# Performance work log

Measured on AMD Instinct MI355X. Metric: run time of the kernel, lower is better.

## Reference

```python
import jax, jax.numpy as jnp
import numpy as np

N_NODES = 100000
N_EDGES = 1600000
NFEAT, NHID, NCLASS = 256, 128, 40


def setup_inputs() -> dict:
    key = jax.random.key(0)
    ks = jax.random.split(key, 8)
    x = jax.random.normal(ks[0], (N_NODES, NFEAT), dtype=jnp.float32)
    edge_src = jax.random.randint(ks[1], (N_EDGES,), 0, N_NODES, dtype=jnp.int32)
    edge_dst = jax.random.randint(ks[2], (N_EDGES,), 0, N_NODES, dtype=jnp.int32)
    edge_weight = jax.random.uniform(ks[3], (N_EDGES,), dtype=jnp.float32)
    W1 = jax.random.normal(ks[4], (NFEAT, NHID), dtype=jnp.float32) * (1.0 / np.sqrt(NFEAT))
    b1 = jnp.zeros((NHID,), dtype=jnp.float32)
    W2 = jax.random.normal(ks[5], (NHID, NCLASS), dtype=jnp.float32) * (1.0 / np.sqrt(NHID))
    b2 = jnp.zeros((NCLASS,), dtype=jnp.float32)
    return {"x": x, "edge_src": edge_src, "edge_dst": edge_dst,
            "edge_weight": edge_weight, "W1": W1, "b1": b1, "W2": W2, "b2": b2}


def _spmm(edge_src, edge_dst, edge_weight, h):
    # out[i] = sum_{e: dst[e]==i} w[e] * h[src[e]]  (sparse adj @ h)
    msgs = edge_weight[:, None] * h[edge_src]            # [E, D]
    return jax.ops.segment_sum(msgs, edge_dst, num_segments=N_NODES)


def reference(x, edge_src, edge_dst, edge_weight, W1, b1, W2, b2):
    # GraphConvolution 1: adj @ (x @ W1) + b1, then ReLU
    h = _spmm(edge_src, edge_dst, edge_weight, x @ W1) + b1
    h = jax.nn.relu(h)
    # Dropout(p=0.5) is identity in eval/deterministic reference
    # GraphConvolution 2: adj @ (h @ W2) + b2
    out = _spmm(edge_src, edge_dst, edge_weight, h @ W2) + b2
    return out
```

## Files before the change

kernel.cpp:

```cpp
#include <hip/hip_runtime.h>

#define N_NODES 100000
#define N_EDGES 1600000
#define NFEAT 256
#define NHID 128
#define NCLASS 40

#define NGROUP 8
#define NODES_PER_GROUP 12500
#define NBKT 128
#define NPB 782
#define KPB (NPB * 8)
#define BCAP2 13200
#define EPB2 8192
#define NCH2 ((N_EDGES + EPB2 - 1) / EPB2)
#define NGEMM1 ((N_NODES + 127) / 128)
#define NKEY (N_NODES * 8)

using short8 = __attribute__((ext_vector_type(8))) short;
using f32x4 = __attribute__((ext_vector_type(4))) float;
using i32x4 = __attribute__((ext_vector_type(4))) int;
using i32x2 = __attribute__((ext_vector_type(2))) int;

__device__ inline float blo(unsigned u) { return __uint_as_float(u << 16); }
__device__ inline float bhi(unsigned u) { return __uint_as_float(u & 0xffff0000u); }
__device__ inline unsigned pk2(float a, float b) {
  unsigned x = __float_as_uint(a), y = __float_as_uint(b);
  unsigned lo = (x + 0x7FFFu + ((x >> 16) & 1u)) >> 16;
  unsigned hi = (y + 0x7FFFu + ((y >> 16) & 1u)) >> 16;
  return lo | (hi << 16);
}
__device__ inline unsigned short pk1(float a) {
  unsigned x = __float_as_uint(a);
  return (unsigned short)((x + 0x7FFFu + ((x >> 16) & 1u)) >> 16);
}


__global__ __launch_bounds__(512) void k_fatA(const int* __restrict__ src,
                                              const int* __restrict__ dst,
                                              const float* __restrict__ w,
                                              int* __restrict__ bcnt,
                                              int* __restrict__ bktK,
                                              i32x2* __restrict__ bktSW,
                                              const float* __restrict__ W1,
                                              unsigned short* __restrict__ w1s) {
  int tid = threadIdx.x;
  if (blockIdx.x >= NCH2) {
    int t = (blockIdx.x - NCH2) * 512 + tid;
    if (t < NFEAT * NHID) {
      int k = t >> 7, c = t & 127;
      int idx = (c * 256 + k) ^ ((c & 7) << 3);
      w1s[idx] = pk1(W1[t]);
    }
    return;
  }
  __shared__ int lcnt[NBKT], loff[NBKT], lcur[NBKT], lbase[NBKT];
  __shared__ int eK[EPB2];
  __shared__ i32x2 eSW[EPB2];
  if (tid < NBKT) lcnt[tid] = 0;
  __syncthreads();

  int base_e = blockIdx.x * EPB2;
  int nE = N_EDGES - base_e;
  if (nE > EPB2) nE = EPB2;
  int e0 = base_e + tid * 16;
  int key[16];
  i32x2 sw[16];
  bool full = (tid * 16 + 16 <= nE);
  if (full) {
#pragma unroll
    for (int g = 0; g < 4; g++) {
      i32x4 d4 = __builtin_nontemporal_load((const i32x4*)(dst + e0 + g * 4));
      i32x4 s4 = __builtin_nontemporal_load((const i32x4*)(src + e0 + g * 4));
      f32x4 w4 = __builtin_nontemporal_load((const f32x4*)(w + e0 + g * 4));
      int dd[4] = {d4.x, d4.y, d4.z, d4.w};
      int ss[4] = {s4.x, s4.y, s4.z, s4.w};
      float ww[4] = {w4.x, w4.y, w4.z, w4.w};
#pragma unroll
      for (int i = 0; i < 4; i++) {
        key[g * 4 + i] = dd[i] * 8 + (int)((unsigned)ss[i] / NODES_PER_GROUP);
        sw[g * 4 + i].x = ss[i];
        sw[g * 4 + i].y = __float_as_int(ww[i]);
        atomicAdd(&lcnt[(unsigned)dd[i] / NPB], 1);
      }
    }
  } else {
#pragma unroll
    for (int i = 0; i < 16; i++) {
      int e = tid * 16 + i;
      if (e < nE) {
        int d = dst[base_e + e], s = src[base_e + e];
        float ww = w[base_e + e];
        key[i] = d * 8 + (int)((unsigned)s / NODES_PER_GROUP);
        sw[i].x = s;
        sw[i].y = __float_as_int(ww);
        atomicAdd(&lcnt[(unsigned)d / NPB], 1);
      } else {
        key[i] = -1;
      }
    }
  }
  __syncthreads();
  if (tid < NBKT) loff[tid] = lcnt[tid];
  __syncthreads();
  for (int off = 1; off < NBKT; off <<= 1) {
    int u = (tid < NBKT && tid >= off) ? loff[tid - off] : 0;
    __syncthreads();
    if (tid < NBKT) loff[tid] += u;
    __syncthreads();
  }
  if (tid < NBKT) {
    int excl = loff[tid] - lcnt[tid];
    loff[tid] = excl;
    lcur[tid] = excl;
    lbase[tid] = atomicAdd(&bcnt[tid], lcnt[tid]);
  }
  __syncthreads();
#pragma unroll
  for (int i = 0; i < 16; i++) {
    if (key[i] >= 0) {
      int b = (unsigned)key[i] / KPB;
      int p = atomicAdd(&lcur[b], 1);
      eK[p] = key[i];
      eSW[p] = sw[i];
    }
  }
  __syncthreads();
  int wid = tid >> 6, lane = tid & 63;
  for (int b = wid; b < NBKT; b += 8) {
    int cnt = lcnt[b];
    int l0 = loff[b];
    int gb = lbase[b];
    if (gb + cnt > BCAP2) cnt = BCAP2 - gb;
    size_t g0 = (size_t)b * BCAP2 + gb;
    for (int i = lane; i < cnt; i += 64) {
      bktK[g0 + i] = eK[l0 + i];
      bktSW[g0 + i] = eSW[l0 + i];
    }
  }
}


__global__ __launch_bounds__(256) void k_gemm1(const float* __restrict__ x,
                                               const uint4* __restrict__ w1s,
                                               unsigned* __restrict__ h1u) {
  __shared__ char sB[65536];
  int tid = threadIdx.x;
  {
    uint4* dd = (uint4*)sB;
    for (int i = 0; i < 16; i++) dd[tid + i * 256] = w1s[tid + i * 256];
  }
  __syncthreads();

  int lane = tid & 63, wid = tid >> 6;
  int r16 = lane & 15, kgrp = lane >> 4;
  int rowbase = blockIdx.x * 128 + wid * 32;
  int ra0 = min(rowbase + r16, N_NODES - 1);
  int ra1 = min(rowbase + 16 + r16, N_NODES - 1);

  f32x4 acc[2][8];
#pragma unroll
  for (int m = 0; m < 2; m++)
#pragma unroll
    for (int n = 0; n < 8; n++) acc[m][n] = (f32x4){0.f, 0.f, 0.f, 0.f};

  for (int kt8 = 0; kt8 < 8; kt8++) {
    int k0 = kt8 * 32 + kgrp * 8;
    union { uint4 u; short8 s; } a[2];
#pragma unroll
    for (int m = 0; m < 2; m++) {
      const float* ap = x + (size_t)(m ? ra1 : ra0) * NFEAT + k0;
      float4 v0 = *(const float4*)ap;
      float4 v1 = *(const float4*)(ap + 4);
      a[m].u.x = pk2(v0.x, v0.y);
      a[m].u.y = pk2(v0.z, v0.w);
      a[m].u.z = pk2(v1.x, v1.y);
      a[m].u.w = pk2(v1.z, v1.w);
    }
#pragma unroll
    for (int n = 0; n < 8; n++) {
      int c = 16 * n + r16;
      int off = (c * 512 + k0 * 2) ^ ((c & 7) << 4);
      short8 b = *(const short8*)(sB + off);
      acc[0][n] = __builtin_amdgcn_mfma_f32_16x16x32_bf16(a[0].s, b, acc[0][n], 0, 0, 0);
      acc[1][n] = __builtin_amdgcn_mfma_f32_16x16x32_bf16(a[1].s, b, acc[1][n], 0, 0, 0);
    }
  }

#pragma unroll
  for (int m = 0; m < 2; m++) {
    int rb = rowbase + m * 16 + kgrp * 4;
#pragma unroll
    for (int n = 0; n < 8; n++) {
      f32x4 v = acc[m][n];
#pragma unroll
      for (int j = 0; j < 4; j++) {
        float o = __shfl_xor(v[j], 1);
        int row = rb + j;
        if (!(lane & 1) && row < N_NODES)
          h1u[(size_t)row * 64 + 8 * n + (r16 >> 1)] = pk2(v[j], o);
      }
    }
  }
}


__global__ __launch_bounds__(1024) void k_build(const int* __restrict__ bcnt,
                                                const int* __restrict__ bktK,
                                                const i32x2* __restrict__ bktSW,
                                                int* __restrict__ rp2,
                                                i32x2* __restrict__ esw) {
  __shared__ int lh[KPB];
  __shared__ int partial[1024];
  __shared__ int sc[NBKT];
  __shared__ i32x2 ebuf[BCAP2];

  int b = blockIdx.x;
  int t = threadIdx.x;
  if (t < NBKT) sc[t] = bcnt[t];
  __syncthreads();
  for (int off = 1; off < NBKT; off <<= 1) {
    int u = (t < NBKT && t >= off) ? sc[t - off] : 0;
    __syncthreads();
    if (t < NBKT) sc[t] += u;
    __syncthreads();
  }
  int base = (b == 0) ? 0 : sc[b - 1];
  int cnt = min(bcnt[b], BCAP2);
  const int* kb = bktK + (size_t)b * BCAP2;
  const i32x2* sb = bktSW + (size_t)b * BCAP2;
  int k0 = b * KPB;

  for (int i = t; i < KPB; i += 1024) lh[i] = 0;
  __syncthreads();
  for (int i = t; i < cnt; i += 1024) atomicAdd(&lh[kb[i] - k0], 1);
  __syncthreads();

  int myoff = t * 7;
  int vals[7];
  int s0 = 0;
#pragma unroll
  for (int q = 0; q < 7; q++) {
    int i = myoff + q;
    int v = (i < KPB) ? lh[i] : 0;
    vals[q] = s0;
    s0 += v;
  }
  partial[t] = s0;
  __syncthreads();
  for (int off = 1; off < 1024; off <<= 1) {
    int u = (t >= off) ? partial[t - off] : 0;
    __syncthreads();
    partial[t] += u;
    __syncthreads();
  }
  int excl_base = partial[t] - s0;
  __syncthreads();
#pragma unroll
  for (int q = 0; q < 7; q++) {
    int i = myoff + q;
    if (i < KPB) {
      int e = excl_base + vals[q];
      int gk = k0 + i;
      if (gk < NKEY) rp2[gk] = base + e;
    }
  }
  __syncthreads();
#pragma unroll
  for (int q = 0; q < 7; q++) {
    int i = myoff + q;
    if (i < KPB) lh[i] = excl_base + vals[q];
  }
  if (b == NBKT - 1 && t == 0) rp2[NKEY] = N_EDGES;
  __syncthreads();

  for (int i = t; i < cnt; i += 1024) {
    int lk = kb[i] - k0;
    int pos = atomicAdd(&lh[lk], 1);
    ebuf[pos] = sb[i];
  }
  __syncthreads();

  i32x2* dstp = esw + base;
  for (int i = t; i < cnt; i += 1024) dstp[i] = ebuf[i];
}


__global__ __launch_bounds__(256) void k_spmm1(const unsigned* __restrict__ h1u,
                                               const int* __restrict__ rp2,
                                               const i32x2* __restrict__ esw,
                                               const float* __restrict__ bias1,
                                               unsigned* __restrict__ houtu) {
  int node = (blockIdx.x * 256 + threadIdx.x) >> 6;
  int lane = threadIdx.x & 63;
  if (node >= N_NODES) return;
  int beg = rp2[node * 8], end = rp2[node * 8 + 8];
  float aL0 = 0.f, aL1 = 0.f, aL2 = 0.f, aL3 = 0.f;
  float aH0 = 0.f, aH1 = 0.f, aH2 = 0.f, aH3 = 0.f;
  int j = beg;
  for (; j + 15 < end; j += 16) {
    i32x2 e[16];
#pragma unroll
    for (int q = 0; q < 16; q++) e[q] = esw[j + q];
    unsigned u[16];
#pragma unroll
    for (int q = 0; q < 16; q++) u[q] = h1u[((unsigned)e[q].x << 6) + lane];
#pragma unroll
    for (int q = 0; q < 16; q += 4) {
      float w0 = __int_as_float(e[q].y), w1 = __int_as_float(e[q + 1].y);
      float w2 = __int_as_float(e[q + 2].y), w3 = __int_as_float(e[q + 3].y);
      aL0 = fmaf(w0, blo(u[q]), aL0);     aH0 = fmaf(w0, bhi(u[q]), aH0);
      aL1 = fmaf(w1, blo(u[q + 1]), aL1); aH1 = fmaf(w1, bhi(u[q + 1]), aH1);
      aL2 = fmaf(w2, blo(u[q + 2]), aL2); aH2 = fmaf(w2, bhi(u[q + 2]), aH2);
      aL3 = fmaf(w3, blo(u[q + 3]), aL3); aH3 = fmaf(w3, bhi(u[q + 3]), aH3);
    }
  }
  for (; j + 7 < end; j += 8) {
    i32x2 e0 = esw[j],     e1 = esw[j + 1], e2 = esw[j + 2], e3 = esw[j + 3];
    i32x2 e4 = esw[j + 4], e5 = esw[j + 5], e6 = esw[j + 6], e7 = esw[j + 7];
    unsigned u0 = h1u[((unsigned)e0.x << 6) + lane];
    unsigned u1 = h1u[((unsigned)e1.x << 6) + lane];
    unsigned u2 = h1u[((unsigned)e2.x << 6) + lane];
    unsigned u3 = h1u[((unsigned)e3.x << 6) + lane];
    unsigned u4 = h1u[((unsigned)e4.x << 6) + lane];
    unsigned u5 = h1u[((unsigned)e5.x << 6) + lane];
    unsigned u6 = h1u[((unsigned)e6.x << 6) + lane];
    unsigned u7 = h1u[((unsigned)e7.x << 6) + lane];
    float w0 = __int_as_float(e0.y), w1 = __int_as_float(e1.y);
    float w2 = __int_as_float(e2.y), w3 = __int_as_float(e3.y);
    float w4 = __int_as_float(e4.y), w5 = __int_as_float(e5.y);
    float w6 = __int_as_float(e6.y), w7 = __int_as_float(e7.y);
    aL0 = fmaf(w0, blo(u0), aL0); aH0 = fmaf(w0, bhi(u0), aH0);
    aL1 = fmaf(w1, blo(u1), aL1); aH1 = fmaf(w1, bhi(u1), aH1);
    aL2 = fmaf(w2, blo(u2), aL2); aH2 = fmaf(w2, bhi(u2), aH2);
    aL3 = fmaf(w3, blo(u3), aL3); aH3 = fmaf(w3, bhi(u3), aH3);
    aL0 = fmaf(w4, blo(u4), aL0); aH0 = fmaf(w4, bhi(u4), aH0);
    aL1 = fmaf(w5, blo(u5), aL1); aH1 = fmaf(w5, bhi(u5), aH1);
    aL2 = fmaf(w6, blo(u6), aL2); aH2 = fmaf(w6, bhi(u6), aH2);
    aL3 = fmaf(w7, blo(u7), aL3); aH3 = fmaf(w7, bhi(u7), aH3);
  }
  for (; j + 3 < end; j += 4) {
    i32x2 e0 = esw[j], e1 = esw[j + 1], e2 = esw[j + 2], e3 = esw[j + 3];
    unsigned u0 = h1u[((unsigned)e0.x << 6) + lane];
    unsigned u1 = h1u[((unsigned)e1.x << 6) + lane];
    unsigned u2 = h1u[((unsigned)e2.x << 6) + lane];
    unsigned u3 = h1u[((unsigned)e3.x << 6) + lane];
    float w0 = __int_as_float(e0.y), w1 = __int_as_float(e1.y);
    float w2 = __int_as_float(e2.y), w3 = __int_as_float(e3.y);
    aL0 = fmaf(w0, blo(u0), aL0); aH0 = fmaf(w0, bhi(u0), aH0);
    aL1 = fmaf(w1, blo(u1), aL1); aH1 = fmaf(w1, bhi(u1), aH1);
    aL2 = fmaf(w2, blo(u2), aL2); aH2 = fmaf(w2, bhi(u2), aH2);
    aL3 = fmaf(w3, blo(u3), aL3); aH3 = fmaf(w3, bhi(u3), aH3);
  }
  for (; j < end; j++) {
    i32x2 e0 = esw[j];
    unsigned u0 = h1u[((unsigned)e0.x << 6) + lane];
    float w0 = __int_as_float(e0.y);
    aL0 = fmaf(w0, blo(u0), aL0); aH0 = fmaf(w0, bhi(u0), aH0);
  }
  float r0 = (aL0 + aL1) + (aL2 + aL3) + bias1[2 * lane];
  float r1 = (aH0 + aH1) + (aH2 + aH3) + bias1[2 * lane + 1];
  houtu[(size_t)node * 64 + lane] = pk2(fmaxf(r0, 0.f), fmaxf(r1, 0.f));
}


__global__ __launch_bounds__(256) void k_gemm2(const unsigned* __restrict__ h_u,
                                               const float* __restrict__ W2,
                                               unsigned short* __restrict__ h2b) {
  __shared__ float hs[32][132];
  __shared__ float w2t[40][132];
  int tid = threadIdx.x;
  int row0 = blockIdx.x * 32;
  for (int i = tid; i < NHID * NCLASS; i += 256) {
    int k = i / NCLASS, c = i % NCLASS;
    w2t[c][k] = W2[i];
  }
  for (int i = tid; i < 2048; i += 256) {
    int r = i >> 6, c = i & 63;
    unsigned u = h_u[(size_t)(row0 + r) * 64 + c];
    hs[r][2 * c] = blo(u);
    hs[r][2 * c + 1] = bhi(u);
  }
  __syncthreads();
  int r = tid >> 3;
  int c0 = (tid & 7) * 5;
  float acc[5] = {0, 0, 0, 0, 0};
  for (int k = 0; k < NHID; k += 4) {
    float4 a = *(float4*)&hs[r][k];
#pragma unroll
    for (int j = 0; j < 5; j++) {
      float4 b = *(float4*)&w2t[c0 + j][k];
      acc[j] += a.x * b.x + a.y * b.y + a.z * b.z + a.w * b.w;
    }
  }
#pragma unroll
  for (int j = 0; j < 5; j++) h2b[(size_t)(row0 + r) * NCLASS + c0 + j] = pk1(acc[j]);
}


__global__ __launch_bounds__(256) void k_spmm2(const unsigned* __restrict__ h2u,
                                               const int* __restrict__ rp2,
                                               const i32x2* __restrict__ esw,
                                               const float* __restrict__ b2,
                                               float* __restrict__ out) {
  int node = (blockIdx.x * 256 + threadIdx.x) >> 6;
  int lane = threadIdx.x & 63;
  if (node >= N_NODES) return;
  int beg = rp2[node * 8], end = rp2[node * 8 + 8];
  int g = lane / 20;
  int jj = lane - g * 20;
  float aA0 = 0.f, aB0 = 0.f, aA1 = 0.f, aB1 = 0.f;
  if (g < 3) {
    int e = beg + g;
    for (; e + 3 < end; e += 6) {
      i32x2 p0 = esw[e];
      i32x2 p1 = esw[e + 3];
      unsigned u0 = h2u[(size_t)p0.x * 20 + jj];
      unsigned u1 = h2u[(size_t)p1.x * 20 + jj];
      float w0 = __int_as_float(p0.y), w1 = __int_as_float(p1.y);
      aA0 = fmaf(w0, blo(u0), aA0); aB0 = fmaf(w0, bhi(u0), aB0);
      aA1 = fmaf(w1, blo(u1), aA1); aB1 = fmaf(w1, bhi(u1), aB1);
    }
    if (e < end) {
      i32x2 p0 = esw[e];
      unsigned u0 = h2u[(size_t)p0.x * 20 + jj];
      float w0 = __int_as_float(p0.y);
      aA0 = fmaf(w0, blo(u0), aA0); aB0 = fmaf(w0, bhi(u0), aB0);
    }
  }
  float accA = aA0 + aA1, accB = aB0 + aB1;
  float tA = accA + __shfl(accA, lane + 20) + __shfl(accA, lane + 40);
  float tB = accB + __shfl(accB, lane + 20) + __shfl(accB, lane + 40);
  if (lane < 20) {
    float2 o = make_float2(tA + b2[2 * lane], tB + b2[2 * lane + 1]);
    *(float2*)&out[(size_t)node * NCLASS + 2 * lane] = o;
  }
}

extern "C" void kernel_launch(void* const* d_in, const int* in_sizes, int n_in,
                              void* d_out, int out_size, void* d_ws, size_t ws_size,
                              hipStream_t stream) {
  const float* x = (const float*)d_in[0];
  const int* src_in = (const int*)d_in[1];
  const int* dst_in = (const int*)d_in[2];
  const float* w_in = (const float*)d_in[3];
  const float* W1 = (const float*)d_in[4];
  const float* b1 = (const float*)d_in[5];
  const float* W2 = (const float*)d_in[6];
  const float* b2 = (const float*)d_in[7];
  float* out = (float*)d_out;

  unsigned short* h1b = (unsigned short*)d_ws;
  unsigned* hbuf = (unsigned*)(h1b + (size_t)N_NODES * NHID);
  unsigned short* h2b = (unsigned short*)(hbuf + (size_t)N_NODES * 64);
  i32x2* esw = (i32x2*)(h2b + (size_t)N_NODES * NCLASS);
  i32x2* bktSW = esw + N_EDGES;
  int* bktK = (int*)(bktSW + (size_t)NBKT * BCAP2);
  int* bcnt = bktK + (size_t)NBKT * BCAP2;
  int* rp2 = bcnt + NBKT;
  unsigned short* w1s = (unsigned short*)(rp2 + NKEY + 4);

  hipMemsetAsync(bcnt, 0, NBKT * sizeof(int), stream);
  k_fatA<<<NCH2 + 64, 512, 0, stream>>>(src_in, dst_in, w_in, bcnt, bktK, bktSW, W1, w1s);
  k_gemm1<<<NGEMM1, 256, 0, stream>>>(x, (const uint4*)w1s, (unsigned*)h1b);
  k_build<<<NBKT, 1024, 0, stream>>>(bcnt, bktK, bktSW, rp2, esw);

  k_spmm1<<<(N_NODES + 3) / 4, 256, 0, stream>>>((const unsigned*)h1b, rp2, esw, b1, hbuf);
  k_gemm2<<<N_NODES / 32, 256, 0, stream>>>(hbuf, W2, h2b);
  k_spmm2<<<(N_NODES + 3) / 4, 256, 0, stream>>>((const unsigned*)h2b, rp2, esw, b2, out);
}
```

Before: 224.3 us.

## Fuse second-layer GEMM into first SpMM epilogue

The first SpMM kernel now keeps each node's ReLU'd hidden row in shared memory and immediately multiplies it by W2, which is staged into shared memory per block. It writes packed bf16 class logits directly, eliminating the separate GEMM kernel and the intermediate hidden-feature buffer round trip through global memory. In exchange, every block reloads the full 20KB W2 matrix and uses more shared memory, which may reduce occupancy in the gather-bound SpMM.

```diff
diff --git a/kernel.cpp b/kernel.cpp
--- a/kernel.cpp
+++ b/kernel.cpp
@@ -286,13 +286,24 @@
 }
 
 
-__global__ __launch_bounds__(256) void k_spmm1(const unsigned* __restrict__ h1u,
-                                               const int* __restrict__ rp2,
-                                               const i32x2* __restrict__ esw,
-                                               const float* __restrict__ bias1,
-                                               unsigned* __restrict__ houtu) {
-  int node = (blockIdx.x * 256 + threadIdx.x) >> 6;
-  int lane = threadIdx.x & 63;
+__global__ __launch_bounds__(256) void k_spmm1f(const unsigned* __restrict__ h1u,
+                                                const int* __restrict__ rp2,
+                                                const i32x2* __restrict__ esw,
+                                                const float* __restrict__ bias1,
+                                                const float* __restrict__ W2,
+                                                unsigned* __restrict__ h2u) {
+  __shared__ float w2s[NHID * NCLASS];
+  __shared__ float hrow[4][NHID];
+  int tid = threadIdx.x;
+  {
+    float4* d4 = (float4*)w2s;
+    const float4* s4 = (const float4*)W2;
+    for (int i = tid; i < NHID * NCLASS / 4; i += 256) d4[i] = s4[i];
+  }
+  __syncthreads();
+
+  int node = (blockIdx.x * 256 + tid) >> 6;
+  int lane = tid & 63, wid = tid >> 6;
   if (node >= N_NODES) return;
   int beg = rp2[node * 8], end = rp2[node * 8 + 8];
   float aL0 = 0.f, aL1 = 0.f, aL2 = 0.f, aL3 = 0.f;
@@ -360,41 +371,23 @@
   }
   float r0 = (aL0 + aL1) + (aL2 + aL3) + bias1[2 * lane];
   float r1 = (aH0 + aH1) + (aH2 + aH3) + bias1[2 * lane + 1];
-  houtu[(size_t)node * 64 + lane] = pk2(fmaxf(r0, 0.f), fmaxf(r1, 0.f));
-}
-
-
-__global__ __launch_bounds__(256) void k_gemm2(const unsigned* __restrict__ h_u,
-                                               const float* __restrict__ W2,
-                                               unsigned short* __restrict__ h2b) {
-  __shared__ float hs[32][132];
-  __shared__ float w2t[40][132];
-  int tid = threadIdx.x;
-  int row0 = blockIdx.x * 32;
-  for (int i = tid; i < NHID * NCLASS; i += 256) {
-    int k = i / NCLASS, c = i % NCLASS;
-    w2t[c][k] = W2[i];
-  }
-  for (int i = tid; i < 2048; i += 256) {
-    int r = i >> 6, c = i & 63;
-    unsigned u = h_u[(size_t)(row0 + r) * 64 + c];
-    hs[r][2 * c] = blo(u);
-    hs[r][2 * c + 1] = bhi(u);
-  }
-  __syncthreads();
-  int r = tid >> 3;
-  int c0 = (tid & 7) * 5;
-  float acc[5] = {0, 0, 0, 0, 0};
+  hrow[wid][2 * lane] = fmaxf(r0, 0.f);
+  hrow[wid][2 * lane + 1] = fmaxf(r1, 0.f);
+
+  int c = lane < NCLASS ? lane : NCLASS - 1;
+  float acc = 0.f;
+#pragma unroll 8
   for (int k = 0; k < NHID; k += 4) {
-    float4 a = *(float4*)&hs[r][k];
-#pragma unroll
-    for (int j = 0; j < 5; j++) {
-      float4 b = *(float4*)&w2t[c0 + j][k];
-      acc[j] += a.x * b.x + a.y * b.y + a.z * b.z + a.w * b.w;
-    }
-  }
-#pragma unroll
-  for (int j = 0; j < 5; j++) h2b[(size_t)(row0 + r) * NCLASS + c0 + j] = pk1(acc[j]);
+    float4 h4 = *(const float4*)&hrow[wid][k];
+    acc = fmaf(h4.x, w2s[k * NCLASS + c], acc);
+    acc = fmaf(h4.y, w2s[(k + 1) * NCLASS + c], acc);
+    acc = fmaf(h4.z, w2s[(k + 2) * NCLASS + c], acc);
+    acc = fmaf(h4.w, w2s[(k + 3) * NCLASS + c], acc);
+  }
+  int sl0 = lane < 20 ? 2 * lane : 0;
+  float v0 = __shfl(acc, sl0);
+  float v1 = __shfl(acc, sl0 + 1);
+  if (lane < 20) h2u[(size_t)node * 20 + lane] = pk2(v0, v1);
 }
 
 
@@ -451,9 +444,8 @@
   float* out = (float*)d_out;
 
   unsigned short* h1b = (unsigned short*)d_ws;
-  unsigned* hbuf = (unsigned*)(h1b + (size_t)N_NODES * NHID);
-  unsigned short* h2b = (unsigned short*)(hbuf + (size_t)N_NODES * 64);
-  i32x2* esw = (i32x2*)(h2b + (size_t)N_NODES * NCLASS);
+  unsigned* h2u = (unsigned*)(h1b + (size_t)N_NODES * NHID);
+  i32x2* esw = (i32x2*)(h2u + (size_t)N_NODES * 20);
   i32x2* bktSW = esw + N_EDGES;
   int* bktK = (int*)(bktSW + (size_t)NBKT * BCAP2);
   int* bcnt = bktK + (size_t)NBKT * BCAP2;
@@ -465,7 +457,6 @@
   k_gemm1<<<NGEMM1, 256, 0, stream>>>(x, (const uint4*)w1s, (unsigned*)h1b);
   k_build<<<NBKT, 1024, 0, stream>>>(bcnt, bktK, bktSW, rp2, esw);
 
-  k_spmm1<<<(N_NODES + 3) / 4, 256, 0, stream>>>((const unsigned*)h1b, rp2, esw, b1, hbuf);
-  k_gemm2<<<N_NODES / 32, 256, 0, stream>>>(hbuf, W2, h2b);
-  k_spmm2<<<(N_NODES + 3) / 4, 256, 0, stream>>>((const unsigned*)h2b, rp2, esw, b2, out);
-}
+  k_spmm1f<<<(N_NODES + 3) / 4, 256, 0, stream>>>((const unsigned*)h1b, rp2, esw, b1, W2, h2u);
+  k_spmm2<<<(N_NODES + 3) / 4, 256, 0, stream>>>((const unsigned*)h2u, rp2, esw, b2, out);
+}
```

New measurement: 247.4 us. 1.1x slower.
